# Performance work log

Hardware: AMD Instinct MI355X
Metric: run time of the kernel (lower is better)

Reference implementation:

```python
import jax, jax.numpy as jnp
import numpy as np

EPS = 1e-5


def _gcn_norm(edge_index, num_nodes):
    # PyG GCNConv default: add self-loops, then sym-normalize D^-1/2 A_hat D^-1/2
    row, col = edge_index[0], edge_index[1]
    loop = jnp.arange(num_nodes, dtype=edge_index.dtype)
    row = jnp.concatenate([row, loop])
    col = jnp.concatenate([col, loop])
    ones = jnp.ones(row.shape[0], dtype=jnp.float32)
    deg = jax.ops.segment_sum(ones, col, num_segments=num_nodes)
    dinv = jnp.where(deg > 0, jax.lax.rsqrt(deg), 0.0)
    norm = dinv[row] * dinv[col]
    return row, col, norm


def _layer_norm(x, gamma, beta):
    mu = jnp.mean(x, axis=-1, keepdims=True)
    var = jnp.mean(jnp.square(x - mu), axis=-1, keepdims=True)
    return (x - mu) * jax.lax.rsqrt(var + EPS) * gamma + beta


def setup_inputs() -> dict:
    key = jax.random.key(0)
    N, E, IN, H, L = 50000, 800000, 16, 64, 3
    ks = jax.random.split(key, 8)
    x = jax.random.normal(ks[0], (N, IN), dtype=jnp.float32)
    edge_index = jax.random.randint(ks[1], (2, E), 0, N, dtype=jnp.int64)
    s = 1.0 / np.sqrt(H)
    W_in = jax.random.normal(ks[2], (IN, H), dtype=jnp.float32) / np.sqrt(IN)
    b_in = jnp.zeros((H,), jnp.float32)
    W_conv = jax.random.normal(ks[3], (L, H, H), dtype=jnp.float32) * s
    b_conv = jnp.zeros((L, H), jnp.float32)
    gamma = jnp.ones((L, H), jnp.float32)
    beta = jnp.zeros((L, H), jnp.float32)
    W_out = jax.random.normal(ks[4], (H, 1), dtype=jnp.float32) * s
    b_out = jnp.zeros((1,), jnp.float32)
    return {"x": x, "edge_index": edge_index, "W_in": W_in, "b_in": b_in,
            "W_conv": W_conv, "b_conv": b_conv, "gamma": gamma, "beta": beta,
            "W_out": W_out, "b_out": b_out}


def reference(x, edge_index, W_in, b_in, W_conv, b_conv, gamma, beta, W_out, b_out):
    N = x.shape[0]
    row, col, norm = _gcn_norm(edge_index, N)
    h = jax.nn.relu(x @ W_in + b_in)  # [N, H]
    num_layers = W_conv.shape[0]
    for i in range(num_layers):
        residual = h
        t = h @ W_conv[i]                              # transform
        msg = t[row] * norm[:, None]                   # gather + scale [E+N, H]
        agg = jax.ops.segment_sum(msg, col, num_segments=N) + b_conv[i]
        h = _layer_norm(agg, gamma[i], beta[i])
        h = jax.nn.relu(h)                             # dropout = identity (eval)
        h = h + residual
    out = h @ W_out + b_out                            # [N, 1]
    return out.reshape(-1)
```

## Files before the change

### kernel.cpp

```cpp
#include <hip/hip_runtime.h>

#define EPS 1e-5f
#define CAP 64
#define RS 256
#define BCAP 32
#define TN 8

typedef unsigned short ushort_t;
typedef unsigned char u8;
typedef unsigned int u32;
typedef __attribute__((ext_vector_type(2))) float vf2;


__device__ __forceinline__ ushort_t pk_fp8(float a, float b) {
    return (ushort_t)(__builtin_amdgcn_cvt_pk_fp8_f32(a, b, 0, false) & 0xFFFF);
}
__device__ __forceinline__ vf2 unpk_lo(u32 v) {
    return (vf2)__builtin_amdgcn_cvt_pk_f32_fp8((int)v, false);
}
__device__ __forceinline__ vf2 unpk_hi(u32 v) {
    return (vf2)__builtin_amdgcn_cvt_pk_f32_fp8((int)v, true);
}


__global__ void k_p1_mlp(const int* __restrict__ row, const int* __restrict__ col,
                         u8* __restrict__ blkCnt, u32* __restrict__ seg,
                         int e, int nr, int nblk, int p1Blocks, int mlpBlocks,
                         const float* __restrict__ x, const float* __restrict__ Win,
                         const float* __restrict__ bin, float2* __restrict__ h2,
                         ushort_t* __restrict__ ts, int n) {
    __shared__ u32 lcnt[256];
    if (blockIdx.x < (unsigned)p1Blocks) {
        for (int j = threadIdx.x; j < 256; j += 256) lcnt[j] = 0;
        __syncthreads();
        int base = blockIdx.x * 1024 + threadIdx.x;
#pragma unroll
        for (int k = 0; k < 4; ++k) {
            int i = base + k * 256;
            if (i < e) {
                int c = col[i];
                int rw = row[i];
                int r = c >> 8;
                u32 rank = atomicAdd(&lcnt[r], 1u);
                if (rank < BCAP)
                    seg[((size_t)r * nblk + blockIdx.x) * BCAP + rank] =
                        ((u32)c << 16) | (u32)rw;
            }
        }
        __syncthreads();
        for (int j = threadIdx.x; j < nr; j += 256)
            blkCnt[(size_t)j * nblk + blockIdx.x] = (u8)min(lcnt[j], (u32)BCAP);
        return;
    }
    int b = blockIdx.x - p1Blocks;
    if (b >= mlpBlocks) {
        if (threadIdx.x < 16) ((u32*)ts)[(size_t)n * 16 + threadIdx.x] = 0;
        return;
    }
    int wv = threadIdx.x >> 6, lane = threadIdx.x & 63;
    int node = b * 4 + wv;
    if (node >= n) return;
    int m = lane & 31;
    float ax = bin[m], ay = bin[m + 32];
    const float* xr = x + (size_t)node * 16;
#pragma unroll
    for (int k = 0; k < 16; ++k) {
        float xv = xr[k];
        ax += xv * Win[k * 64 + m];
        ay += xv * Win[k * 64 + m + 32];
    }
    ax = fmaxf(ax, 0.0f);
    ay = fmaxf(ay, 0.0f);
    if (lane < 32) h2[(size_t)node * 32 + m] = make_float2(ax, ay);
}


__global__ void k_p2(const u8* __restrict__ blkCnt, const u32* __restrict__ seg,
                     ushort_t* __restrict__ bRowF, int* __restrict__ cnt,
                     int nblk, int n) {
    __shared__ ushort_t bkt[RS * CAP];
    __shared__ u32 lcnt[RS];
    int r = blockIdx.x;
    u32 fillv = ((u32)n << 16) | (u32)n;
    u32* bw = (u32*)bkt;
    for (int j = threadIdx.x; j < RS * CAP / 2; j += blockDim.x) bw[j] = fillv;
    for (int j = threadIdx.x; j < RS; j += blockDim.x) lcnt[j] = 0;
    __syncthreads();
    for (int b = threadIdx.x; b < nblk; b += blockDim.x) {
        int cb = blkCnt[(size_t)r * nblk + b];
        const u32* s = seg + ((size_t)r * nblk + b) * BCAP;
        for (int j = 0; j < cb; ++j) {
            u32 p = s[j];
            int cl = (p >> 16) & (RS - 1);
            u32 slot = atomicAdd(&lcnt[cl], 1u);
            if (slot < CAP) bkt[(cl << 6) + slot] = (ushort_t)(p & 0xFFFF);
        }
    }
    __syncthreads();
    int nodeBase = r << 8;
    int nNodes = min(RS, n - nodeBase);
    if (nNodes <= 0) return;
    u32* dst = (u32*)(bRowF + ((size_t)nodeBase << 6));
    const u32* src = (const u32*)bkt;
    for (int j = threadIdx.x; j < nNodes * 32; j += blockDim.x) dst[j] = src[j];
    for (int j = threadIdx.x; j < nNodes; j += blockDim.x)
        cnt[nodeBase + j] = (int)lcnt[j];
}


__global__ __launch_bounds__(256, 4)
void k_transform(const float2* __restrict__ h2, const int* __restrict__ cnt,
                 const float* __restrict__ W, ushort_t* __restrict__ ts, int n) {
    int wv = threadIdx.x >> 6, lane = threadIdx.x & 63;
    int wid = blockIdx.x * 4 + wv;
    int n0 = wid * TN;
    if (n0 >= n) return;
    int nEnd = min(n0 + TN, n);
    float w[64];
#pragma unroll
    for (int j = 0; j < 64; ++j) {
        int k = (j >> 1) + ((j & 1) << 5);
        w[j] = W[k * 64 + lane];
    }
    int m = lane & 31;
    for (int node = n0; node < nEnd; ++node) {
        int nu = __builtin_amdgcn_readfirstlane(node);
        const float4* yr4 = (const float4*)(h2 + (size_t)nu * 32);
        float a0 = 0.f, a1 = 0.f, a2 = 0.f, a3 = 0.f;
#pragma unroll
        for (int j4 = 0; j4 < 16; ++j4) {
            float4 y = yr4[j4];
            a0 = fmaf(y.x, w[4 * j4 + 0], a0);
            a1 = fmaf(y.y, w[4 * j4 + 1], a1);
            a2 = fmaf(y.z, w[4 * j4 + 2], a2);
            a3 = fmaf(y.w, w[4 * j4 + 3], a3);
        }
        float dv = rsqrtf((float)(cnt[nu] + 1));
        float t = ((a0 + a1) + (a2 + a3)) * dv;
        float other = __shfl_xor(t, 32);
        if (lane < 32) ts[(size_t)nu * 32 + m] = pk_fp8(t, other);
    }
}


__global__ __launch_bounds__(256, 4)
void k_gather(const int* __restrict__ cnt, const ushort_t* __restrict__ bRow,
              const ushort_t* __restrict__ ts,
              const float* __restrict__ bc, const float* __restrict__ gm,
              const float* __restrict__ bt, float2* __restrict__ h2, int n,
              const float* __restrict__ Wout, const float* __restrict__ bout,
              float* __restrict__ out, int do_out) {
    int wv = threadIdx.x >> 6, lane = threadIdx.x & 63;
    int qtr = lane >> 4, q = lane & 15;
    int node = blockIdx.x * 16 + wv * 4 + qtr;
    bool alive = node < n;
    int nl = alive ? node : 0;

    int deg = cnt[nl];
    float dvv = rsqrtf((float)(deg + 1));
    int gneed = alive ? ((min(deg, CAP) + 7) >> 3) : 0;
    int g1 = max(gneed, __shfl_xor(gneed, 16));
    int gmax = __builtin_amdgcn_readfirstlane(max(g1, __shfl_xor(g1, 32)));

    const char* tsb = (const char*)ts;
    u32 qoff = (u32)q << 2;
    u32 selfw = *(const u32*)(tsb + (((u32)nl << 6) | qoff));
    float4 hv = *(const float4*)((const float*)h2 + (size_t)nl * 64 + 4 * q);
    const uint4* bq = (const uint4*)(bRow + ((size_t)nl << 6));

    vf2 a0 = {0.f, 0.f}, a1 = {0.f, 0.f};
    uint4 bw = bq[0];
    for (int g = 0; g < gmax; ++g) {
        uint4 bwn = bq[min(g + 1, 7)];
        u32 o0 = ((bw.x & 0xFFFFu) << 6) | qoff;
        u32 o1 = ((bw.x >> 16) << 6) | qoff;
        u32 o2 = ((bw.y & 0xFFFFu) << 6) | qoff;
        u32 o3 = ((bw.y >> 16) << 6) | qoff;
        u32 o4 = ((bw.z & 0xFFFFu) << 6) | qoff;
        u32 o5 = ((bw.z >> 16) << 6) | qoff;
        u32 o6 = ((bw.w & 0xFFFFu) << 6) | qoff;
        u32 o7 = ((bw.w >> 16) << 6) | qoff;
        u32 v0 = *(const u32*)(tsb + o0);
        u32 v1 = *(const u32*)(tsb + o1);
        u32 v2 = *(const u32*)(tsb + o2);
        u32 v3 = *(const u32*)(tsb + o3);
        u32 v4 = *(const u32*)(tsb + o4);
        u32 v5 = *(const u32*)(tsb + o5);
        u32 v6 = *(const u32*)(tsb + o6);
        u32 v7 = *(const u32*)(tsb + o7);
        a0 += unpk_lo(v0); a1 += unpk_hi(v0);
        a0 += unpk_lo(v1); a1 += unpk_hi(v1);
        a0 += unpk_lo(v2); a1 += unpk_hi(v2);
        a0 += unpk_lo(v3); a1 += unpk_hi(v3);
        a0 += unpk_lo(v4); a1 += unpk_hi(v4);
        a0 += unpk_lo(v5); a1 += unpk_hi(v5);
        a0 += unpk_lo(v6); a1 += unpk_hi(v6);
        a0 += unpk_lo(v7); a1 += unpk_hi(v7);
        bw = bwn;
    }
    vf2 s0 = unpk_lo(selfw), s1 = unpk_hi(selfw);
    float2 bc0 = *(const float2*)(bc + 2 * q);
    float2 bc1 = *(const float2*)(bc + 32 + 2 * q);
    float vx0 = (a0.x + s0.x) * dvv + bc0.x;
    float vx1 = (a1.x + s1.x) * dvv + bc0.y;
    float vy0 = (a0.y + s0.y) * dvv + bc1.x;
    float vy1 = (a1.y + s1.y) * dvv + bc1.y;
    float s = (vx0 + vx1) + (vy0 + vy1);
#pragma unroll
    for (int off = 8; off; off >>= 1) s += __shfl_xor(s, off, 16);
    float mu = s * (1.0f / 64.0f);
    float d0 = vx0 - mu, d1 = vx1 - mu, d2 = vy0 - mu, d3 = vy1 - mu;
    float qq = (d0 * d0 + d1 * d1) + (d2 * d2 + d3 * d3);
#pragma unroll
    for (int off = 8; off; off >>= 1) qq += __shfl_xor(qq, off, 16);
    float inv = rsqrtf(qq * (1.0f / 64.0f) + EPS);
    float2 g0 = *(const float2*)(gm + 2 * q);
    float2 g1v = *(const float2*)(gm + 32 + 2 * q);
    float2 b0 = *(const float2*)(bt + 2 * q);
    float2 b1 = *(const float2*)(bt + 32 + 2 * q);
    float y00 = fmaxf(d0 * inv * g0.x + b0.x, 0.0f) + hv.x;
    float y01 = fmaxf(d1 * inv * g0.y + b0.y, 0.0f) + hv.z;
    float y10 = fmaxf(d2 * inv * g1v.x + b1.x, 0.0f) + hv.y;
    float y11 = fmaxf(d3 * inv * g1v.y + b1.y, 0.0f) + hv.w;
    if (!do_out) {
        if (alive)
            *(float4*)((float*)h2 + (size_t)nl * 64 + 4 * q) =
                make_float4(y00, y10, y01, y11);
    } else {
        float2 w0 = *(const float2*)(Wout + 2 * q);
        float2 w1 = *(const float2*)(Wout + 32 + 2 * q);
        float o = (y00 * w0.x + y01 * w0.y) + (y10 * w1.x + y11 * w1.y);
#pragma unroll
        for (int off = 8; off; off >>= 1) o += __shfl_xor(o, off, 16);
        if (alive && q == 0) out[nl] = o + bout[0];
    }
}

extern "C" void kernel_launch(void* const* d_in, const int* in_sizes, int n_in,
                              void* d_out, int out_size, void* d_ws, size_t ws_size,
                              hipStream_t stream) {
    const float* x     = (const float*)d_in[0];
    const int*   eidx  = (const int*)d_in[1];
    const float* Win   = (const float*)d_in[2];
    const float* bin   = (const float*)d_in[3];
    const float* Wconv = (const float*)d_in[4];
    const float* bconv = (const float*)d_in[5];
    const float* gamma = (const float*)d_in[6];
    const float* beta  = (const float*)d_in[7];
    const float* Wout  = (const float*)d_in[8];
    const float* bout  = (const float*)d_in[9];
    float* out = (float*)d_out;

    const int N = in_sizes[0] / 16;
    const int E = in_sizes[1] / 2;
    const int L = in_sizes[4] / (64 * 64);

    const int* row = eidx;
    const int* col = eidx + E;

    char* ws = (char*)d_ws;
    size_t off = 0;
    auto alloc = [&](size_t bytes) -> void* {
        size_t p = off;
        off += (bytes + 255) & ~(size_t)255;
        return (void*)(ws + p);
    };
    const int NR   = (N + RS - 1) / RS;
    const int NBLK = (E + 1023) / 1024;
    int*      cnt    = (int*)alloc((size_t)(N + 1) * 4);
    ushort_t* bRowF  = (ushort_t*)alloc((size_t)(N + RS) * CAP * 2);
    u8*       blkCnt = (u8*)alloc((size_t)NR * NBLK);
    u32*      seg    = (u32*)alloc((size_t)NR * NBLK * BCAP * 4);
    ushort_t* ts     = (ushort_t*)alloc((size_t)(N + 1) * 32 * 2);
    float2*   h2     = (float2*)alloc((size_t)N * 32 * 8);
    (void)ws_size;

    const int BT = 256;
    int gN64 = (N + 3) / 4;
    int gG   = (N + 15) / 16;
    int gT   = ((N + TN - 1) / TN + 3) / 4;

    k_p1_mlp<<<NBLK + gN64 + 1, BT, 0, stream>>>(row, col, blkCnt, seg, E, NR, NBLK,
                                                 NBLK, gN64, x, Win, bin, h2, ts, N);
    k_p2<<<NR, 1024, 0, stream>>>(blkCnt, seg, bRowF, cnt, NBLK, N);

    for (int l = 0; l < L; ++l) {
        const float* Wc = Wconv + (size_t)l * 64 * 64;
        const float* bc = bconv + (size_t)l * 64;
        const float* gmv = gamma + (size_t)l * 64;
        const float* bt = beta + (size_t)l * 64;
        int last = (l == L - 1);
        k_transform<<<gT, BT, 0, stream>>>(h2, cnt, Wc, ts, N);
        k_gather<<<gG, BT, 0, stream>>>(cnt, bRowF, ts, bc, gmv, bt, h2, N,
                                        Wout, bout, out, last);
    }
}
```

Baseline: 199.4 us.

## Fuse per-layer transform into bucket build and previous gather epilogue

Removes the standalone k_transform launches. The first layer's feature transform now runs inside the bucket-building kernel, using the shared-memory counts. Later layers' transforms are computed in the gather kernel's epilogue from LDS-staged outputs, with ping-pong fp8 buffers. This drops three kernel launches and the re-read of h between kernels, but the gather kernel now reloads W from global per k-step and does more work per wave, which may add register and latency pressure.

```diff
diff --git a/kernel.cpp b/kernel.cpp
--- a/kernel.cpp
+++ b/kernel.cpp
@@ -4,7 +4,6 @@
 #define CAP 64
 #define RS 256
 #define BCAP 32
-#define TN 8
 
 typedef unsigned short ushort_t;
 typedef unsigned char u8;
@@ -28,7 +27,8 @@
                          int e, int nr, int nblk, int p1Blocks, int mlpBlocks,
                          const float* __restrict__ x, const float* __restrict__ Win,
                          const float* __restrict__ bin, float2* __restrict__ h2,
-                         ushort_t* __restrict__ ts, int n) {
+                         ushort_t* __restrict__ tsA, ushort_t* __restrict__ tsB,
+                         int n) {
     __shared__ u32 lcnt[256];
     if (blockIdx.x < (unsigned)p1Blocks) {
         for (int j = threadIdx.x; j < 256; j += 256) lcnt[j] = 0;
@@ -54,7 +54,10 @@
     }
     int b = blockIdx.x - p1Blocks;
     if (b >= mlpBlocks) {
-        if (threadIdx.x < 16) ((u32*)ts)[(size_t)n * 16 + threadIdx.x] = 0;
+        if (threadIdx.x < 16) {
+            ((u32*)tsA)[(size_t)n * 16 + threadIdx.x] = 0;
+            ((u32*)tsB)[(size_t)n * 16 + threadIdx.x] = 0;
+        }
         return;
     }
     int wv = threadIdx.x >> 6, lane = threadIdx.x & 63;
@@ -75,15 +78,16 @@
 }
 
 
-__global__ void k_p2(const u8* __restrict__ blkCnt, const u32* __restrict__ seg,
-                     ushort_t* __restrict__ bRowF, int* __restrict__ cnt,
-                     int nblk, int n) {
+__global__ void k_p2t(const u8* __restrict__ blkCnt, const u32* __restrict__ seg,
+                      ushort_t* __restrict__ bRowF, int* __restrict__ cnt,
+                      const float2* __restrict__ h2, const float* __restrict__ W0,
+                      ushort_t* __restrict__ tsA, int nblk, int n) {
     __shared__ ushort_t bkt[RS * CAP];
     __shared__ u32 lcnt[RS];
     int r = blockIdx.x;
     u32 fillv = ((u32)n << 16) | (u32)n;
-    u32* bw = (u32*)bkt;
-    for (int j = threadIdx.x; j < RS * CAP / 2; j += blockDim.x) bw[j] = fillv;
+    u32* bw_ = (u32*)bkt;
+    for (int j = threadIdx.x; j < RS * CAP / 2; j += blockDim.x) bw_[j] = fillv;
     for (int j = threadIdx.x; j < RS; j += blockDim.x) lcnt[j] = 0;
     __syncthreads();
     for (int b = threadIdx.x; b < nblk; b += blockDim.x) {
@@ -99,32 +103,25 @@
     __syncthreads();
     int nodeBase = r << 8;
     int nNodes = min(RS, n - nodeBase);
-    if (nNodes <= 0) return;
-    u32* dst = (u32*)(bRowF + ((size_t)nodeBase << 6));
-    const u32* src = (const u32*)bkt;
-    for (int j = threadIdx.x; j < nNodes * 32; j += blockDim.x) dst[j] = src[j];
-    for (int j = threadIdx.x; j < nNodes; j += blockDim.x)
-        cnt[nodeBase + j] = (int)lcnt[j];
-}
-
-
-__global__ __launch_bounds__(256, 4)
-void k_transform(const float2* __restrict__ h2, const int* __restrict__ cnt,
-                 const float* __restrict__ W, ushort_t* __restrict__ ts, int n) {
+    if (nNodes > 0) {
+        u32* dst = (u32*)(bRowF + ((size_t)nodeBase << 6));
+        const u32* src = (const u32*)bkt;
+        for (int j = threadIdx.x; j < nNodes * 32; j += blockDim.x) dst[j] = src[j];
+        for (int j = threadIdx.x; j < nNodes; j += blockDim.x)
+            cnt[nodeBase + j] = (int)lcnt[j];
+    }
     int wv = threadIdx.x >> 6, lane = threadIdx.x & 63;
-    int wid = blockIdx.x * 4 + wv;
-    int n0 = wid * TN;
-    if (n0 >= n) return;
-    int nEnd = min(n0 + TN, n);
     float w[64];
 #pragma unroll
     for (int j = 0; j < 64; ++j) {
         int k = (j >> 1) + ((j & 1) << 5);
-        w[j] = W[k * 64 + lane];
+        w[j] = W0[k * 64 + lane];
     }
     int m = lane & 31;
-    for (int node = n0; node < nEnd; ++node) {
-        int nu = __builtin_amdgcn_readfirstlane(node);
+    int lim = min(16, nNodes - wv * 16);
+    for (int i = 0; i < lim; ++i) {
+        int ln = wv * 16 + i;
+        int nu = __builtin_amdgcn_readfirstlane(nodeBase + ln);
         const float4* yr4 = (const float4*)(h2 + (size_t)nu * 32);
         float a0 = 0.f, a1 = 0.f, a2 = 0.f, a3 = 0.f;
 #pragma unroll
@@ -135,21 +132,23 @@
             a2 = fmaf(y.z, w[4 * j4 + 2], a2);
             a3 = fmaf(y.w, w[4 * j4 + 3], a3);
         }
-        float dv = rsqrtf((float)(cnt[nu] + 1));
+        float dv = rsqrtf((float)(lcnt[ln] + 1));
         float t = ((a0 + a1) + (a2 + a3)) * dv;
         float other = __shfl_xor(t, 32);
-        if (lane < 32) ts[(size_t)nu * 32 + m] = pk_fp8(t, other);
+        if (lane < 32) tsA[(size_t)nu * 32 + m] = pk_fp8(t, other);
     }
 }
 
 
 __global__ __launch_bounds__(256, 4)
-void k_gather(const int* __restrict__ cnt, const ushort_t* __restrict__ bRow,
-              const ushort_t* __restrict__ ts,
-              const float* __restrict__ bc, const float* __restrict__ gm,
-              const float* __restrict__ bt, float2* __restrict__ h2, int n,
-              const float* __restrict__ Wout, const float* __restrict__ bout,
-              float* __restrict__ out, int do_out) {
+void k_gather_f(const int* __restrict__ cnt, const ushort_t* __restrict__ bRow,
+                const ushort_t* __restrict__ tsi,
+                const float* __restrict__ bc, const float* __restrict__ gm,
+                const float* __restrict__ bt, float2* __restrict__ h2, int n,
+                const float* __restrict__ Wn, ushort_t* __restrict__ tso,
+                const float* __restrict__ Wout, const float* __restrict__ bout,
+                float* __restrict__ out, int last) {
+    __shared__ float ysm[4][4][64];
     int wv = threadIdx.x >> 6, lane = threadIdx.x & 63;
     int qtr = lane >> 4, q = lane & 15;
     int node = blockIdx.x * 16 + wv * 4 + qtr;
@@ -162,7 +161,7 @@
     int g1 = max(gneed, __shfl_xor(gneed, 16));
     int gmax = __builtin_amdgcn_readfirstlane(max(g1, __shfl_xor(g1, 32)));
 
-    const char* tsb = (const char*)ts;
+    const char* tsb = (const char*)tsi;
     u32 qoff = (u32)q << 2;
     u32 selfw = *(const u32*)(tsb + (((u32)nl << 6) | qoff));
     float4 hv = *(const float4*)((const float*)h2 + (size_t)nl * 64 + 4 * q);
@@ -222,10 +221,47 @@
     float y01 = fmaxf(d1 * inv * g0.y + b0.y, 0.0f) + hv.z;
     float y10 = fmaxf(d2 * inv * g1v.x + b1.x, 0.0f) + hv.y;
     float y11 = fmaxf(d3 * inv * g1v.y + b1.y, 0.0f) + hv.w;
-    if (!do_out) {
+
+    if (!last) {
         if (alive)
             *(float4*)((float*)h2 + (size_t)nl * 64 + 4 * q) =
                 make_float4(y00, y10, y01, y11);
+        float* yw = &ysm[wv][qtr][0];
+        yw[2 * q] = y00; yw[2 * q + 1] = y01;
+        yw[2 * q + 32] = y10; yw[2 * q + 33] = y11;
+        __builtin_amdgcn_wave_barrier();
+        const float* ya = &ysm[wv][0][0];
+        const float* yb = &ysm[wv][1][0];
+        const float* yc = &ysm[wv][2][0];
+        const float* yd = &ysm[wv][3][0];
+        float t0 = 0.f, t1 = 0.f, t2 = 0.f, t3 = 0.f;
+#pragma unroll
+        for (int k4 = 0; k4 < 16; ++k4) {
+            float4 fa = *(const float4*)(ya + 4 * k4);
+            float4 fb = *(const float4*)(yb + 4 * k4);
+            float4 fc = *(const float4*)(yc + 4 * k4);
+            float4 fd = *(const float4*)(yd + 4 * k4);
+            float w0 = Wn[(4 * k4 + 0) * 64 + lane];
+            float w1 = Wn[(4 * k4 + 1) * 64 + lane];
+            float w2 = Wn[(4 * k4 + 2) * 64 + lane];
+            float w3 = Wn[(4 * k4 + 3) * 64 + lane];
+            t0 = fmaf(fa.x, w0, fmaf(fa.y, w1, fmaf(fa.z, w2, fmaf(fa.w, w3, t0))));
+            t1 = fmaf(fb.x, w0, fmaf(fb.y, w1, fmaf(fb.z, w2, fmaf(fb.w, w3, t1))));
+            t2 = fmaf(fc.x, w0, fmaf(fc.y, w1, fmaf(fc.z, w2, fmaf(fc.w, w3, t2))));
+            t3 = fmaf(fd.x, w0, fmaf(fd.y, w1, fmaf(fd.z, w2, fmaf(fd.w, w3, t3))));
+        }
+        float dv0 = __shfl(dvv, 0), dv1 = __shfl(dvv, 16);
+        float dv2 = __shfl(dvv, 32), dv3 = __shfl(dvv, 48);
+        t0 *= dv0; t1 *= dv1; t2 *= dv2; t3 *= dv3;
+        float o0 = __shfl_xor(t0, 32), o1 = __shfl_xor(t1, 32);
+        float o2 = __shfl_xor(t2, 32), o3 = __shfl_xor(t3, 32);
+        if (lane < 32) {
+            int nb0 = blockIdx.x * 16 + wv * 4;
+            if (nb0 + 0 < n) tso[((size_t)(nb0 + 0) << 5) + lane] = pk_fp8(t0, o0);
+            if (nb0 + 1 < n) tso[((size_t)(nb0 + 1) << 5) + lane] = pk_fp8(t1, o1);
+            if (nb0 + 2 < n) tso[((size_t)(nb0 + 2) << 5) + lane] = pk_fp8(t2, o2);
+            if (nb0 + 3 < n) tso[((size_t)(nb0 + 3) << 5) + lane] = pk_fp8(t3, o3);
+        }
     } else {
         float2 w0 = *(const float2*)(Wout + 2 * q);
         float2 w1 = *(const float2*)(Wout + 32 + 2 * q);
@@ -271,27 +307,30 @@
     ushort_t* bRowF  = (ushort_t*)alloc((size_t)(N + RS) * CAP * 2);
     u8*       blkCnt = (u8*)alloc((size_t)NR * NBLK);
     u32*      seg    = (u32*)alloc((size_t)NR * NBLK * BCAP * 4);
-    ushort_t* ts     = (ushort_t*)alloc((size_t)(N + 1) * 32 * 2);
+    ushort_t* tsA    = (ushort_t*)alloc((size_t)(N + 1) * 32 * 2);
+    ushort_t* tsB    = (ushort_t*)alloc((size_t)(N + 1) * 32 * 2);
     float2*   h2     = (float2*)alloc((size_t)N * 32 * 8);
     (void)ws_size;
 
     const int BT = 256;
-    int gN64 = (N + 3) / 4;
+    int gMLP = (N + 3) / 4;
     int gG   = (N + 15) / 16;
-    int gT   = ((N + TN - 1) / TN + 3) / 4;
-
-    k_p1_mlp<<<NBLK + gN64 + 1, BT, 0, stream>>>(row, col, blkCnt, seg, E, NR, NBLK,
-                                                 NBLK, gN64, x, Win, bin, h2, ts, N);
-    k_p2<<<NR, 1024, 0, stream>>>(blkCnt, seg, bRowF, cnt, NBLK, N);
-
+
+    k_p1_mlp<<<NBLK + gMLP + 1, BT, 0, stream>>>(row, col, blkCnt, seg, E, NR, NBLK,
+                                                 NBLK, gMLP, x, Win, bin, h2,
+                                                 tsA, tsB, N);
+    k_p2t<<<NR, 1024, 0, stream>>>(blkCnt, seg, bRowF, cnt, h2, Wconv, tsA, NBLK, N);
+
+    ushort_t* ti = tsA;
+    ushort_t* to = tsB;
     for (int l = 0; l < L; ++l) {
-        const float* Wc = Wconv + (size_t)l * 64 * 64;
         const float* bc = bconv + (size_t)l * 64;
         const float* gmv = gamma + (size_t)l * 64;
         const float* bt = beta + (size_t)l * 64;
         int last = (l == L - 1);
-        k_transform<<<gT, BT, 0, stream>>>(h2, cnt, Wc, ts, N);
-        k_gather<<<gG, BT, 0, stream>>>(cnt, bRowF, ts, bc, gmv, bt, h2, N,
-                                        Wout, bout, out, last);
-    }
-}
+        const float* Wn = Wconv + (size_t)(last ? l : l + 1) * 4096;
+        k_gather_f<<<gG, BT, 0, stream>>>(cnt, bRowF, ti, bc, gmv, bt, h2, N,
+                                          Wn, to, Wout, bout, out, last);
+        ushort_t* tmp = ti; ti = to; to = tmp;
+    }
+}
```

New measurement: 183.0 us. 1.09x faster.
